# Performance work log

Hardware: AMD Instinct MI355X
Metric: run time of the kernel (lower is better)

Reference implementation:

```python
import jax, jax.numpy as jnp
import numpy as np

N = 100000   # nodes
E = 1600000  # edges
NF, EF = 128, 16      # node_features, edge_features
NFIL, EFIL = 64, 32   # node_filters, edge_filters
C = 16                # classes


def setup_inputs() -> dict:
    key = jax.random.key(0)
    ks = jax.random.split(key, 12)
    s = 0.1
    return {
        "x": jax.random.normal(ks[0], (N, NF), jnp.float32),
        "edge_index": jax.random.randint(ks[1], (2, E), 0, N),
        "edge_x": jax.random.normal(ks[2], (E, EF), jnp.float32),
        # edge MLP params
        "W1": jax.random.normal(ks[3], (EF, EFIL), jnp.float32) * s,
        "b1": jnp.zeros((EFIL,), jnp.float32),
        "W2": jax.random.normal(ks[4], (EFIL, 1), jnp.float32) * s,
        "b2": jnp.zeros((1,), jnp.float32),
        # GCN layer params
        "Wc1": jax.random.normal(ks[5], (NF, NFIL), jnp.float32) * s,
        "bc1": jnp.zeros((NFIL,), jnp.float32),
        "Wc2": jax.random.normal(ks[6], (NFIL, C), jnp.float32) * s,
        "bc2": jnp.zeros((C,), jnp.float32),
    }


def gcn_conv(x, src, tgt, w, W, b, n):
    # PyG GCNConv with edge_weight: x @ W, symmetric norm, scatter-add, + bias.
    x = x @ W                                             # [n, out]
    deg = jax.ops.segment_sum(w, tgt, num_segments=n)     # weighted degree incl. self-loops
    dinv = jnp.where(deg > 0, jax.lax.rsqrt(deg), 0.0)
    norm = dinv[src] * w * dinv[tgt]                      # [E+n]
    out = jax.ops.segment_sum(norm[:, None] * x[src], tgt, num_segments=n)
    return out + b


def reference(x, edge_index, edge_x, W1, b1, W2, b2, Wc1, bc1, Wc2, bc2):
    # edge MLP -> scalar attention weight per edge
    h = jax.nn.relu(edge_x @ W1 + b1)
    ew = jax.nn.sigmoid(h @ W2 + b2).reshape(-1)          # [E]
    src, tgt = edge_index[0], edge_index[1]
    # add self-loops with weight 1 (as GCNConv does internally)
    loop = jnp.arange(N)
    src_f = jnp.concatenate([src, loop])
    tgt_f = jnp.concatenate([tgt, loop])
    ew_f = jnp.concatenate([ew, jnp.ones((N,), ew.dtype)])
    h1 = jax.nn.relu(gcn_conv(x, src_f, tgt_f, ew_f, Wc1, bc1, N))
    # dropout omitted: eval mode (F.dropout is identity when training=False)
    h2 = gcn_conv(h1, src_f, tgt_f, ew_f, Wc2, bc2, N)
    return jax.nn.log_softmax(h2, axis=1)
```

## Files before the change

kernel.cpp:

```cpp
#include <hip/hip_runtime.h>
#include <math.h>

#define NFD 128
#define EF_ 16
#define EFIL 32
#define NFIL 64
#define CLS 16

typedef unsigned int uint;
typedef unsigned long long ull;
typedef unsigned short ushort;

__device__ inline void fma4(float4& a, float s, const float4& w) {
  a.x = fmaf(s, w.x, a.x); a.y = fmaf(s, w.y, a.y);
  a.z = fmaf(s, w.z, a.z); a.w = fmaf(s, w.w, a.w);
}

__device__ inline uint bf16_rn(float f) {
  uint u = __float_as_uint(f);
  return (u + 0x7FFFu + ((u >> 16) & 1u)) >> 16;
}
__device__ inline float entw(uint lo) {
  return __uint_as_float((lo >> 17) << 16);
}

__global__ __launch_bounds__(256) void edge_gemm_kernel(
    const float* __restrict__ edge_x, const int* __restrict__ ei,
    const float* __restrict__ W1, const float* __restrict__ b1,
    const float* __restrict__ W2, const float* __restrict__ b2,
    int* __restrict__ head, ull* __restrict__ nextbuf, int E,
    const float* __restrict__ x, const float* __restrict__ Wc1,
    uint* __restrict__ xwb, int n, int NBG) {
  extern __shared__ __align__(16) char smem[];
  int t = threadIdx.x;
  int bid = blockIdx.x;
  int gq = (bid + 1) / 7;
  bool is_gemm = ((bid + 1) % 7) == 0;

  if (is_gemm) {
    float* sW = (float*)smem;
    for (int idx = t; idx < NFD * NFIL / 4; idx += 256)
      reinterpret_cast<float4*>(sW)[idx] = reinterpret_cast<const float4*>(Wc1)[idx];
    __syncthreads();
    int tc = t & 15;
    int tr = t >> 4;
    int nrb = (n + 31) >> 5;
    const float4* sW4 = reinterpret_cast<const float4*>(sW);
    for (int rb = gq - 1; rb < nrb; rb += NBG) {
      int r0 = rb * 32 + tr * 2;
      int r1 = r0 + 1;
      int c0 = r0 < n ? r0 : n - 1;
      int c1 = r1 < n ? r1 : n - 1;
      const float4* xr0 = reinterpret_cast<const float4*>(x + (size_t)c0 * NFD);
      const float4* xr1 = reinterpret_cast<const float4*>(x + (size_t)c1 * NFD);
      float4 a0 = {0, 0, 0, 0}, a1 = {0, 0, 0, 0};
      #pragma unroll 4
      for (int k4 = 0; k4 < NFD / 4; k4++) {
        float4 xa = xr0[k4];
        float4 xb = xr1[k4];
        float4 w0 = sW4[(k4*4+0)*16 + tc];
        float4 w1 = sW4[(k4*4+1)*16 + tc];
        float4 w2 = sW4[(k4*4+2)*16 + tc];
        float4 w3 = sW4[(k4*4+3)*16 + tc];
        fma4(a0, xa.x, w0); fma4(a0, xa.y, w1); fma4(a0, xa.z, w2); fma4(a0, xa.w, w3);
        fma4(a1, xb.x, w0); fma4(a1, xb.y, w1); fma4(a1, xb.z, w2); fma4(a1, xb.w, w3);
      }
      if (r0 < n) {
        uint2 o = {bf16_rn(a0.x) | (bf16_rn(a0.y) << 16),
                   bf16_rn(a0.z) | (bf16_rn(a0.w) << 16)};
        reinterpret_cast<uint2*>(xwb + (size_t)r0 * 32)[tc] = o;
      }
      if (r1 < n) {
        uint2 o = {bf16_rn(a1.x) | (bf16_rn(a1.y) << 16),
                   bf16_rn(a1.z) | (bf16_rn(a1.w) << 16)};
        reinterpret_cast<uint2*>(xwb + (size_t)r1 * 32)[tc] = o;
      }
    }
    return;
  }

  int eidx = bid - gq;
  float* sW1 = (float*)smem;
  float* sb1 = sW1 + EF_ * EFIL;
  float* sW2 = sb1 + EFIL;
  float* sb2 = sW2 + EFIL;
  for (int idx = t; idx < EF_ * EFIL / 4; idx += 256)
    reinterpret_cast<float4*>(sW1)[idx] = reinterpret_cast<const float4*>(W1)[idx];
  if (t < EFIL) { sb1[t] = b1[t]; sW2[t] = W2[t]; }
  if (t == 64) sb2[0] = b2[0];
  __syncthreads();
  int e = eidx * 256 + t;
  if (e >= E) return;
  int sv = ei[e], tg = ei[(size_t)E + e];
  int old = atomicExch(&head[(size_t)tg * 8 + (eidx & 7)], e);
  const float4* ex4 = reinterpret_cast<const float4*>(edge_x) + (size_t)e * (EF_ / 4);
  float ex[EF_];
  #pragma unroll
  for (int q = 0; q < EF_ / 4; q++) {
    float4 v = ex4[q];
    ex[4*q+0] = v.x; ex[4*q+1] = v.y; ex[4*q+2] = v.z; ex[4*q+3] = v.w;
  }
  float acc[EFIL];
  #pragma unroll
  for (int j = 0; j < EFIL; j++) acc[j] = sb1[j];
  #pragma unroll
  for (int k = 0; k < EF_; k++) {
    float xk = ex[k];
    #pragma unroll
    for (int j4 = 0; j4 < EFIL / 4; j4++) {
      float4 w = reinterpret_cast<const float4*>(sW1)[k * (EFIL/4) + j4];
      acc[4*j4+0] = fmaf(xk, w.x, acc[4*j4+0]);
      acc[4*j4+1] = fmaf(xk, w.y, acc[4*j4+1]);
      acc[4*j4+2] = fmaf(xk, w.z, acc[4*j4+2]);
      acc[4*j4+3] = fmaf(xk, w.w, acc[4*j4+3]);
    }
  }
  float s = sb2[0];
  #pragma unroll
  for (int j = 0; j < EFIL; j++) s = fmaf(fmaxf(acc[j], 0.f), sW2[j], s);
  float sig = 1.0f / (1.0f + __expf(-s));
  uint lo = ((bf16_rn(sig) & 0x7FFFu) << 17) | (uint)sv;
  nextbuf[e] = ((ull)(uint)old << 32) | lo;
}

__global__ __launch_bounds__(256) void walk_kernel(
    const int* __restrict__ head, const ull* __restrict__ nextbuf,
    uint* __restrict__ slotc, int* __restrict__ grp_cnt,
    float* __restrict__ dinv, int caprows, int n) {
  int i = blockIdx.x * blockDim.x + threadIdx.x;
  if (i >= n) return;
  int4 ha = *reinterpret_cast<const int4*>(head + (size_t)i * 8);
  int4 hb = *reinterpret_cast<const int4*>(head + (size_t)i * 8 + 4);
  int ev0 = ha.x, ev1 = ha.y, ev2 = ha.z, ev3 = ha.w;
  int ev4 = hb.x, ev5 = hb.y, ev6 = hb.z, ev7 = hb.w;
  int cnt = 0;
  float sum = 0.f;
  bool any = ev0 >= 0 || ev1 >= 0 || ev2 >= 0 || ev3 >= 0 ||
             ev4 >= 0 || ev5 >= 0 || ev6 >= 0 || ev7 >= 0;
  while (any) {
    ull v0 = 0, v1 = 0, v2 = 0, v3 = 0, v4 = 0, v5 = 0, v6 = 0, v7 = 0;
    if (ev0 >= 0) v0 = nextbuf[ev0];
    if (ev1 >= 0) v1 = nextbuf[ev1];
    if (ev2 >= 0) v2 = nextbuf[ev2];
    if (ev3 >= 0) v3 = nextbuf[ev3];
    if (ev4 >= 0) v4 = nextbuf[ev4];
    if (ev5 >= 0) v5 = nextbuf[ev5];
    if (ev6 >= 0) v6 = nextbuf[ev6];
    if (ev7 >= 0) v7 = nextbuf[ev7];
    #define STEP(EV, VV)                                              \
    if (EV >= 0) {                                                    \
      uint lo = (uint)VV; sum += entw(lo);                            \
      if (cnt < caprows) slotc[(size_t)cnt * n + i] = lo;             \
      cnt++; EV = (int)(uint)(VV >> 32);                              \
    }
    STEP(ev0, v0) STEP(ev1, v1) STEP(ev2, v2) STEP(ev3, v3)
    STEP(ev4, v4) STEP(ev5, v5) STEP(ev6, v6) STEP(ev7, v7)
    #undef STEP
    any = ev0 >= 0 || ev1 >= 0 || ev2 >= 0 || ev3 >= 0 ||
          ev4 >= 0 || ev5 >= 0 || ev6 >= 0 || ev7 >= 0;
  }
  grp_cnt[i] = min(cnt, caprows);
  dinv[i] = rsqrtf(1.0f + sum);
}

__global__ __launch_bounds__(256) void agg1_fused_kernel(
    const int* __restrict__ grp_cnt, const uint* __restrict__ slotc,
    const float* __restrict__ dinv, const uint* __restrict__ xwb,
    const float* __restrict__ bc1, const float* __restrict__ Wc2,
    ushort* __restrict__ ywb, int n) {
  __shared__ float sh[16][NFIL + 4];
  __shared__ float sW2[NFIL * CLS];
  __shared__ float sb1[NFIL];
  int t = threadIdx.x;
  for (int i = t; i < NFIL * CLS; i += 256) sW2[i] = Wc2[i];
  if (t < NFIL) sb1[t] = bc1[t];
  __syncthreads();
  int r = t >> 4;
  int node = blockIdx.x * 16 + r;
  int f4 = t & 15;
  bool ok = node < n;
  int nd = ok ? node : 0;
  int cnt = ok ? grp_cnt[nd] : 0;
  const uint2* xw2 = reinterpret_cast<const uint2*>(xwb);
  float d = ok ? dinv[nd] : 0.f;
  uint2 g = xw2[(size_t)nd * 16 + f4];
  float4 acc = {d * __uint_as_float(g.x << 16),
                d * __uint_as_float(g.x & 0xFFFF0000u),
                d * __uint_as_float(g.y << 16),
                d * __uint_as_float(g.y & 0xFFFF0000u)};
  #define A1STEP(VV)                                                  \
  {                                                                   \
    int s_ = VV & 0x1FFFF;                                            \
    float w_ = entw(VV) * dinv[s_];                                   \
    uint2 g_ = xw2[(size_t)s_ * 16 + f4];                             \
    acc.x = fmaf(w_, __uint_as_float(g_.x << 16), acc.x);             \
    acc.y = fmaf(w_, __uint_as_float(g_.x & 0xFFFF0000u), acc.y);     \
    acc.z = fmaf(w_, __uint_as_float(g_.y << 16), acc.z);             \
    acc.w = fmaf(w_, __uint_as_float(g_.y & 0xFFFF0000u), acc.w);     \
  }
  int p = 0;
  for (; p + 3 < cnt; p += 4) {
    uint v0 = slotc[(size_t)p * n + nd];
    uint v1 = slotc[(size_t)(p + 1) * n + nd];
    uint v2 = slotc[(size_t)(p + 2) * n + nd];
    uint v3 = slotc[(size_t)(p + 3) * n + nd];
    A1STEP(v0) A1STEP(v1) A1STEP(v2) A1STEP(v3)
  }
  for (; p < cnt; p++) {
    uint v0 = slotc[(size_t)p * n + nd];
    A1STEP(v0)
  }
  #undef A1STEP
  sh[r][4*f4 + 0] = fmaxf(fmaf(d, acc.x, sb1[4*f4 + 0]), 0.f);
  sh[r][4*f4 + 1] = fmaxf(fmaf(d, acc.y, sb1[4*f4 + 1]), 0.f);
  sh[r][4*f4 + 2] = fmaxf(fmaf(d, acc.z, sb1[4*f4 + 2]), 0.f);
  sh[r][4*f4 + 3] = fmaxf(fmaf(d, acc.w, sb1[4*f4 + 3]), 0.f);
  __syncthreads();
  {
    int j = t & 15;
    float o = 0.f;
    #pragma unroll
    for (int k = 0; k < NFIL; k++) o = fmaf(sh[r][k], sW2[k * CLS + j], o);
    if (ok) ywb[(size_t)node * CLS + j] = (ushort)bf16_rn(d * o);
  }
}

__global__ __launch_bounds__(256) void agg2_fused_kernel(
    const int* __restrict__ grp_cnt, const uint* __restrict__ slotc,
    const float* __restrict__ dinv, const ushort* __restrict__ ywb,
    const float* __restrict__ bc2, float* __restrict__ out, int n) {
  __shared__ float sb2[CLS];
  int t = threadIdx.x;
  if (t < CLS) sb2[t] = bc2[t];
  __syncthreads();
  int node = blockIdx.x * 16 + (t >> 4);
  int j = t & 15;
  bool ok = node < n;
  int nd = ok ? node : 0;
  int cnt = ok ? grp_cnt[nd] : 0;
  float d = ok ? dinv[nd] : 0.f;
  float acc = __uint_as_float((uint)ywb[(size_t)nd * CLS + j] << 16);
  #define A2STEP(VV)                                                       \
  {                                                                        \
    int s_ = VV & 0x1FFFF;                                                 \
    acc = fmaf(entw(VV),                                                   \
               __uint_as_float((uint)ywb[(size_t)s_ * CLS + j] << 16),     \
               acc);                                                       \
  }
  int p = 0;
  for (; p + 3 < cnt; p += 4) {
    uint v0 = slotc[(size_t)p * n + nd];
    uint v1 = slotc[(size_t)(p + 1) * n + nd];
    uint v2 = slotc[(size_t)(p + 2) * n + nd];
    uint v3 = slotc[(size_t)(p + 3) * n + nd];
    A2STEP(v0) A2STEP(v1) A2STEP(v2) A2STEP(v3)
  }
  for (; p < cnt; p++) {
    uint v0 = slotc[(size_t)p * n + nd];
    A2STEP(v0)
  }
  #undef A2STEP
  float v = fmaf(d, acc, sb2[j]);
  float m = v;
  m = fmaxf(m, __shfl_xor(m, 1, 16));
  m = fmaxf(m, __shfl_xor(m, 2, 16));
  m = fmaxf(m, __shfl_xor(m, 4, 16));
  m = fmaxf(m, __shfl_xor(m, 8, 16));
  float ex = __expf(v - m);
  float ssum = ex;
  ssum += __shfl_xor(ssum, 1, 16);
  ssum += __shfl_xor(ssum, 2, 16);
  ssum += __shfl_xor(ssum, 4, 16);
  ssum += __shfl_xor(ssum, 8, 16);
  if (ok) out[(size_t)node * CLS + j] = (v - m) - __logf(ssum);
}

extern "C" void kernel_launch(void* const* d_in, const int* in_sizes, int n_in,
                              void* d_out, int out_size, void* d_ws, size_t ws_size,
                              hipStream_t stream) {
  const float* x      = (const float*)d_in[0];
  const int*   ei     = (const int*)d_in[1];
  const float* edge_x = (const float*)d_in[2];
  const float* W1     = (const float*)d_in[3];
  const float* b1     = (const float*)d_in[4];
  const float* W2     = (const float*)d_in[5];
  const float* b2     = (const float*)d_in[6];
  const float* Wc1    = (const float*)d_in[7];
  const float* bc1    = (const float*)d_in[8];
  const float* Wc2    = (const float*)d_in[9];
  const float* bc2    = (const float*)d_in[10];
  float* outp = (float*)d_out;
  int n = in_sizes[0] / NFD;
  int E = in_sizes[1] / 2;

  int cap = 48;
  while (cap > 32 && 8.0 * E + (double)n * (200.0 + 4.0 * cap) > (double)ws_size)
    cap -= 8;

  char* base = (char*)d_ws;
  int* head = (int*)base;            base += (size_t)n * 32;
  ull* nextbuf = (ull*)base;         base += (size_t)E * 8;
  uint* slotc = (uint*)base;         base += (size_t)n * cap * 4;
  int* grp_cnt = (int*)base;         base += (size_t)n * 4;
  float* dinv = (float*)base;        base += (size_t)n * 4;
  uint* xwb = (uint*)base;           base += (size_t)n * 128;
  ushort* ywb = (ushort*)base;

  int NBE = (E + 255) / 256;
  int T = NBE;
  for (int it = 0; it < 8; it++) T = NBE + T / 7;
  while (T - T / 7 < NBE) T++;
  int NBG = T / 7;

  int nblk16 = (n + 15) / 16;
  int nblk256 = (n + 255) / 256;
  hipMemsetAsync(head, 0xFF, (size_t)n * 32, stream);
  edge_gemm_kernel<<<T, 256, 32768, stream>>>(
      edge_x, ei, W1, b1, W2, b2, head, nextbuf, E, x, Wc1, xwb, n, NBG);
  walk_kernel<<<nblk256, 256, 0, stream>>>(head, nextbuf, slotc, grp_cnt, dinv, cap, n);
  agg1_fused_kernel<<<nblk16, 256, 0, stream>>>(grp_cnt, slotc, dinv, xwb, bc1, Wc2, ywb, n);
  agg2_fused_kernel<<<nblk16, 256, 0, stream>>>(grp_cnt, slotc, dinv, ywb, bc2, outp, n);
}
```

Baseline: 195.3 us.

## Run edge MLP and node GEMM in every block instead of separate block roles

Replaces the scheme in which one block in seven did the x@Wc1 GEMM with a Wc1 copy in 32 KB of dynamic LDS. Now every block first does its 256-edge MLP and list insertion, then takes a strided share of the 32-row GEMM tiles. Wc1 is read straight from global memory through the cache instead of being staged in LDS. Dropping the large LDS allocation should raise occupancy and balance work across blocks, at the cost of more global or L1 traffic for the weights.

```diff
diff --git a/kernel.cpp b/kernel.cpp
--- a/kernel.cpp
+++ b/kernel.cpp
@@ -30,23 +30,59 @@
     const float* __restrict__ W2, const float* __restrict__ b2,
     int* __restrict__ head, ull* __restrict__ nextbuf, int E,
     const float* __restrict__ x, const float* __restrict__ Wc1,
-    uint* __restrict__ xwb, int n, int NBG) {
-  extern __shared__ __align__(16) char smem[];
+    uint* __restrict__ xwb, int n) {
+  __shared__ __align__(16) float sW1[EF_ * EFIL];
+  __shared__ float sb1[EFIL];
+  __shared__ float sW2[EFIL];
+  __shared__ float sb2v;
   int t = threadIdx.x;
   int bid = blockIdx.x;
-  int gq = (bid + 1) / 7;
-  bool is_gemm = ((bid + 1) % 7) == 0;
-
-  if (is_gemm) {
-    float* sW = (float*)smem;
-    for (int idx = t; idx < NFD * NFIL / 4; idx += 256)
-      reinterpret_cast<float4*>(sW)[idx] = reinterpret_cast<const float4*>(Wc1)[idx];
-    __syncthreads();
+  for (int idx = t; idx < EF_ * EFIL / 4; idx += 256)
+    reinterpret_cast<float4*>(sW1)[idx] = reinterpret_cast<const float4*>(W1)[idx];
+  if (t < EFIL) { sb1[t] = b1[t]; sW2[t] = W2[t]; }
+  if (t == 64) sb2v = b2[0];
+  __syncthreads();
+
+  int e = bid * 256 + t;
+  if (e < E) {
+    int sv = ei[e], tg = ei[(size_t)E + e];
+    int old = atomicExch(&head[(size_t)tg * 8 + (bid & 7)], e);
+    const float4* ex4 = reinterpret_cast<const float4*>(edge_x) + (size_t)e * (EF_ / 4);
+    float ex[EF_];
+    #pragma unroll
+    for (int q = 0; q < EF_ / 4; q++) {
+      float4 v = ex4[q];
+      ex[4*q+0] = v.x; ex[4*q+1] = v.y; ex[4*q+2] = v.z; ex[4*q+3] = v.w;
+    }
+    float acc[EFIL];
+    #pragma unroll
+    for (int j = 0; j < EFIL; j++) acc[j] = sb1[j];
+    #pragma unroll
+    for (int k = 0; k < EF_; k++) {
+      float xk = ex[k];
+      #pragma unroll
+      for (int j4 = 0; j4 < EFIL / 4; j4++) {
+        float4 w = reinterpret_cast<const float4*>(sW1)[k * (EFIL/4) + j4];
+        acc[4*j4+0] = fmaf(xk, w.x, acc[4*j4+0]);
+        acc[4*j4+1] = fmaf(xk, w.y, acc[4*j4+1]);
+        acc[4*j4+2] = fmaf(xk, w.z, acc[4*j4+2]);
+        acc[4*j4+3] = fmaf(xk, w.w, acc[4*j4+3]);
+      }
+    }
+    float s = sb2v;
+    #pragma unroll
+    for (int j = 0; j < EFIL; j++) s = fmaf(fmaxf(acc[j], 0.f), sW2[j], s);
+    float sig = 1.0f / (1.0f + __expf(-s));
+    uint lo = ((bf16_rn(sig) & 0x7FFFu) << 17) | (uint)sv;
+    nextbuf[e] = ((ull)(uint)old << 32) | lo;
+  }
+
+  {
+    const float4* W4 = reinterpret_cast<const float4*>(Wc1);
     int tc = t & 15;
     int tr = t >> 4;
     int nrb = (n + 31) >> 5;
-    const float4* sW4 = reinterpret_cast<const float4*>(sW);
-    for (int rb = gq - 1; rb < nrb; rb += NBG) {
+    for (int rb = bid; rb < nrb; rb += gridDim.x) {
       int r0 = rb * 32 + tr * 2;
       int r1 = r0 + 1;
       int c0 = r0 < n ? r0 : n - 1;
@@ -58,10 +94,10 @@
       for (int k4 = 0; k4 < NFD / 4; k4++) {
         float4 xa = xr0[k4];
         float4 xb = xr1[k4];
-        float4 w0 = sW4[(k4*4+0)*16 + tc];
-        float4 w1 = sW4[(k4*4+1)*16 + tc];
-        float4 w2 = sW4[(k4*4+2)*16 + tc];
-        float4 w3 = sW4[(k4*4+3)*16 + tc];
+        float4 w0 = W4[(k4*4+0)*16 + tc];
+        float4 w1 = W4[(k4*4+1)*16 + tc];
+        float4 w2 = W4[(k4*4+2)*16 + tc];
+        float4 w3 = W4[(k4*4+3)*16 + tc];
         fma4(a0, xa.x, w0); fma4(a0, xa.y, w1); fma4(a0, xa.z, w2); fma4(a0, xa.w, w3);
         fma4(a1, xb.x, w0); fma4(a1, xb.y, w1); fma4(a1, xb.z, w2); fma4(a1, xb.w, w3);
       }
@@ -76,51 +112,7 @@
         reinterpret_cast<uint2*>(xwb + (size_t)r1 * 32)[tc] = o;
       }
     }
-    return;
-  }
-
-  int eidx = bid - gq;
-  float* sW1 = (float*)smem;
-  float* sb1 = sW1 + EF_ * EFIL;
-  float* sW2 = sb1 + EFIL;
-  float* sb2 = sW2 + EFIL;
-  for (int idx = t; idx < EF_ * EFIL / 4; idx += 256)
-    reinterpret_cast<float4*>(sW1)[idx] = reinterpret_cast<const float4*>(W1)[idx];
-  if (t < EFIL) { sb1[t] = b1[t]; sW2[t] = W2[t]; }
-  if (t == 64) sb2[0] = b2[0];
-  __syncthreads();
-  int e = eidx * 256 + t;
-  if (e >= E) return;
-  int sv = ei[e], tg = ei[(size_t)E + e];
-  int old = atomicExch(&head[(size_t)tg * 8 + (eidx & 7)], e);
-  const float4* ex4 = reinterpret_cast<const float4*>(edge_x) + (size_t)e * (EF_ / 4);
-  float ex[EF_];
-  #pragma unroll
-  for (int q = 0; q < EF_ / 4; q++) {
-    float4 v = ex4[q];
-    ex[4*q+0] = v.x; ex[4*q+1] = v.y; ex[4*q+2] = v.z; ex[4*q+3] = v.w;
-  }
-  float acc[EFIL];
-  #pragma unroll
-  for (int j = 0; j < EFIL; j++) acc[j] = sb1[j];
-  #pragma unroll
-  for (int k = 0; k < EF_; k++) {
-    float xk = ex[k];
-    #pragma unroll
-    for (int j4 = 0; j4 < EFIL / 4; j4++) {
-      float4 w = reinterpret_cast<const float4*>(sW1)[k * (EFIL/4) + j4];
-      acc[4*j4+0] = fmaf(xk, w.x, acc[4*j4+0]);
-      acc[4*j4+1] = fmaf(xk, w.y, acc[4*j4+1]);
-      acc[4*j4+2] = fmaf(xk, w.z, acc[4*j4+2]);
-      acc[4*j4+3] = fmaf(xk, w.w, acc[4*j4+3]);
-    }
-  }
-  float s = sb2[0];
-  #pragma unroll
-  for (int j = 0; j < EFIL; j++) s = fmaf(fmaxf(acc[j], 0.f), sW2[j], s);
-  float sig = 1.0f / (1.0f + __expf(-s));
-  uint lo = ((bf16_rn(sig) & 0x7FFFu) << 17) | (uint)sv;
-  nextbuf[e] = ((ull)(uint)old << 32) | lo;
+  }
 }
 
 __global__ __launch_bounds__(256) void walk_kernel(
@@ -307,16 +299,11 @@
   ushort* ywb = (ushort*)base;
 
   int NBE = (E + 255) / 256;
-  int T = NBE;
-  for (int it = 0; it < 8; it++) T = NBE + T / 7;
-  while (T - T / 7 < NBE) T++;
-  int NBG = T / 7;
-
   int nblk16 = (n + 15) / 16;
   int nblk256 = (n + 255) / 256;
   hipMemsetAsync(head, 0xFF, (size_t)n * 32, stream);
-  edge_gemm_kernel<<<T, 256, 32768, stream>>>(
-      edge_x, ei, W1, b1, W2, b2, head, nextbuf, E, x, Wc1, xwb, n, NBG);
+  edge_gemm_kernel<<<NBE, 256, 0, stream>>>(
+      edge_x, ei, W1, b1, W2, b2, head, nextbuf, E, x, Wc1, xwb, n);
   walk_kernel<<<nblk256, 256, 0, stream>>>(head, nextbuf, slotc, grp_cnt, dinv, cap, n);
   agg1_fused_kernel<<<nblk16, 256, 0, stream>>>(grp_cnt, slotc, dinv, xwb, bc1, Wc2, ywb, n);
   agg2_fused_kernel<<<nblk16, 256, 0, stream>>>(grp_cnt, slotc, dinv, ywb, bc2, outp, n);
```

Measured after the change: 224.3 us. +14.9%, slower.
